# Performance work log

Measured on AMD Instinct MI355X. Metric: run time of the kernel, lower is better.

## Reference

```python
import jax, jax.numpy as jnp
import numpy as np

P, Q, R, H1, H2, PH, B = 32, 32, 8, 128, 64, 16, 8192
PAIRS = P * Q
OUT = PAIRS * R  # X_Z_layer output units


def _pairwise_mask(p, q, r):
    # rows i*q+k correspond to pair (x_i, z_k): connected to x_i and z_k only
    mx = np.zeros((p * q, p), np.float32)
    for i in range(p):
        mx[i * q:(i + 1) * q, i] = 1.0
    mz = np.tile(np.eye(q, dtype=np.float32), (p, 1))
    m = np.concatenate([mx, mz], axis=1)          # [p*q, p+q]
    return np.repeat(m, r, axis=0)                 # [p*q*r, p+q]


def setup_inputs() -> dict:
    key = jax.random.key(0)
    ks = jax.random.split(key, 24)
    rn = lambda k, s, sc=0.1: jax.random.normal(k, s, jnp.float32) * sc
    x = jax.random.normal(ks[0], (B, P), jnp.float32)
    z = jax.random.normal(ks[1], (B, Q), jnp.float32)
    # X_mlp: P -> H1 -> H2 -> 1
    xw1, xb1 = rn(ks[2], (P, H1)), rn(ks[3], (H1,))
    xw2, xb2 = rn(ks[4], (H1, H2)), rn(ks[5], (H2,))
    xw3, xb3 = rn(ks[6], (H2, 1)), rn(ks[7], (1,))
    # Z_mlp: Q -> H1 -> H2 -> 1
    zw1, zb1 = rn(ks[8], (Q, H1)), rn(ks[9], (H1,))
    zw2, zb2 = rn(ks[10], (Q if False else H1, H2)), rn(ks[11], (H2,))
    zw3, zb3 = rn(ks[12], (H2, 1)), rn(ks[13], (1,))
    # masked X_Z_layer: weight pre-multiplied by structured mask (as in __init__)
    mask = jnp.asarray(_pairwise_mask(P, Q, R))    # [OUT, P+Q]
    xzw = (rn(ks[14], (OUT, P + Q)) * mask).T      # [P+Q, OUT]
    xzb = rn(ks[15], (OUT,))
    # 1024 tiny per-pair MLPs: R -> PH (bias) -> 1 (no bias), stacked
    pw1 = rn(ks[16], (PAIRS, R, PH))
    pb1 = rn(ks[17], (PAIRS, PH))
    pw2 = rn(ks[18], (PAIRS, PH))
    return dict(x=x, z=z, xw1=xw1, xb1=xb1, xw2=xw2, xb2=xb2, xw3=xw3, xb3=xb3,
                zw1=zw1, zb1=zb1, zw2=zw2, zb2=zb2, zw3=zw3, zb3=zb3,
                xzw=xzw, xzb=xzb, pw1=pw1, pb1=pb1, pw2=pw2)


def reference(x, z, xw1, xb1, xw2, xb2, xw3, xb3,
              zw1, zb1, zw2, zb2, zw3, zb3, xzw, xzb, pw1, pb1, pw2):
    relu = jax.nn.relu
    # main-effect MLPs
    hx = relu(relu(x @ xw1 + xb1) @ xw2 + xb2)
    out_x = hx @ xw3 + xb3                         # [B,1]
    hz = relu(relu(z @ zw1 + zb1) @ zw2 + zb2)
    out_z = hz @ zw3 + zb3                         # [B,1]
    # masked interaction layer
    xz = jnp.concatenate([x, z], axis=1)           # [B, P+Q]
    h = relu(xz @ xzw + xzb)                       # [B, OUT]
    # all 1024 per-pair MLPs as one batched GEMM
    hp = h.reshape(h.shape[0], PAIRS, R)           # [B, pairs, R]
    t = relu(jnp.einsum('bpr,prh->bph', hp, pw1) + pb1)
    out_xz = jnp.einsum('bph,ph->b', t, pw2)[:, None]  # sum over pairs -> [B,1]
    return out_x + out_z + out_xz
```

## Files before the change

### kernel.cpp

```cpp
#include <hip/hip_runtime.h>

#define B_TOT 8192
#define PP 32
#define QQ 32
#define RR 8
#define H1 128
#define H2 64
#define PHH 16
#define PAIRS 1024
#define OUT_UNITS 8192

#define NBLK_MM 256
#define NBLK_IA 1024

typedef float f32x16 __attribute__((ext_vector_type(16)));
typedef short s16x8  __attribute__((ext_vector_type(8)));

union FragU { s16x8 v; unsigned int u[4]; };

__device__ inline unsigned int pack_bf16(float lo, float hi) {
    unsigned int r;
    asm("v_cvt_pk_bf16_f32 %0, %1, %2" : "=v"(r) : "v"(lo), "v"(hi));
    return r;
}

union SharedU {
    union {
        struct {
            float zT[16][256];
            float4 lwx[32][2];
            float4 lwz[32][2];
            float4 lhb[32][2];
            unsigned lpw1T[33][16][4];
            float lpbw[32][16][2];
        } s;
        float red[256][33];
    } ia;
    struct {
        union {
            float xT[32][68];
            float h1T[128][68];
        };
    } mm;
};

__global__ __launch_bounds__(512, 6) void fused_k(
    const float* __restrict__ x, const float* __restrict__ z,
    const float* __restrict__ xw1, const float* __restrict__ xb1,
    const float* __restrict__ xw2, const float* __restrict__ xb2,
    const float* __restrict__ xw3, const float* __restrict__ xb3,
    const float* __restrict__ zw1, const float* __restrict__ zb1,
    const float* __restrict__ zw2, const float* __restrict__ zb2,
    const float* __restrict__ zw3, const float* __restrict__ zb3,
    const float* __restrict__ xzw, const float* __restrict__ xzb,
    const float* __restrict__ pw1, const float* __restrict__ pb1,
    const float* __restrict__ pw2, float* __restrict__ out)
{
    __shared__ SharedU sh;
    const int bid  = blockIdx.x;
    const int t    = threadIdx.x;
    const int w    = t >> 6;
    const int lane = t & 63;

    if (bid >= NBLK_MM) {
        const int ib    = bid - NBLK_MM;
        const int bx    = ib & 31;
        const int y2    = ib >> 5;
        const int m     = lane & 31;
        const int kh    = lane >> 5;
        const int jj    = m & 15;
        const int cph   = m >> 4;
        const int b0    = bx * 256;
        const int par   = y2 & 1;
        const int i_xb  = y2 & ~1;
        const int k0    = par * 16;
        const int oy0   = 2 * i_xb + par;
        const int oy1   = oy0 + 2;
        const int pair0_0 = oy0 * 16;
        const int pair0_1 = oy1 * 16;

        {
            int row = t >> 1;
            int c8  = (t & 1) * 8;
            const float* src = z + (size_t)(b0 + row) * 32 + k0 + c8;
            float4 a4 = *reinterpret_cast<const float4*>(src);
            float4 b4 = *reinterpret_cast<const float4*>(src + 4);
            sh.ia.s.zT[c8+0][row] = a4.x; sh.ia.s.zT[c8+1][row] = a4.y;
            sh.ia.s.zT[c8+2][row] = a4.z; sh.ia.s.zT[c8+3][row] = a4.w;
            sh.ia.s.zT[c8+4][row] = b4.x; sh.ia.s.zT[c8+5][row] = b4.y;
            sh.ia.s.zT[c8+6][row] = b4.z; sh.ia.s.zT[c8+7][row] = b4.w;
        }
        if (t < 256) {
            int sb  = t >> 7;
            int idx = t & 127;
            int p = idx >> 3, c = idx & 7;
            int gp = (sb ? pair0_1 : pair0_0) + p;
            int pl = sb * 16 + p;
            reinterpret_cast<float*>(sh.ia.s.lwx)[pl*8 + c] = xzw[(size_t)(i_xb + sb) * OUT_UNITS + gp*8 + c];
            reinterpret_cast<float*>(sh.ia.s.lwz)[pl*8 + c] = xzw[(size_t)(32 + k0 + p) * OUT_UNITS + gp*8 + c];
            reinterpret_cast<float*>(sh.ia.s.lhb)[pl*8 + c] = xzb[gp*8 + c];
        }
        {
            int p = t >> 4, j = t & 15;
            int gp = ((p >> 4) ? pair0_1 : pair0_0) + (p & 15);
            float2 bw;
            bw.x = pb1[gp*PHH + j];
            bw.y = pw2[gp*PHH + j];
            *reinterpret_cast<float2*>(sh.ia.s.lpbw[p][j]) = bw;
        }
        #pragma unroll
        for (int it = 0; it < 4; ++it) {
            int idx = t + it * 512;
            int p = idx >> 6, u = (idx >> 4) & 3, j = idx & 15;
            int gp = ((p >> 4) ? pair0_1 : pair0_0) + (p & 15);
            float lo = pw1[(size_t)gp * 128 + (2*u)*16 + j];
            float hi = pw1[(size_t)gp * 128 + (2*u+1)*16 + j];
            sh.ia.s.lpw1T[p][j][u] = pack_bf16(lo, hi);
        }
        if (t < 64) reinterpret_cast<unsigned*>(sh.ia.s.lpw1T[32])[t] = 0u;

        const int bl = w * 32 + m;
        const float2 xv2 = *reinterpret_cast<const float2*>(
            x + (size_t)(b0 + bl) * 32 + i_xb);
        __syncthreads();

        f32x16 acc;
        #pragma unroll
        for (int r = 0; r < 16; ++r) acc[r] = 0.f;

        const bool realB = (kh == cph);

        #pragma unroll 2
        for (int ppl = 0; ppl < 8; ++ppl) {
            const int kA = 2*ppl + kh;
            const int kB = 2*ppl + cph;
            const float zv = sh.ia.s.zT[kA][bl];

            #pragma unroll
            for (int sb = 0; sb < 2; ++sb) {
                const int pAl = sb*16 + kA;
                const int pBl = sb*16 + kB;
                const float xv = sb ? xv2.y : xv2.x;

                const float4 wxa = sh.ia.s.lwx[pAl][0], wxb = sh.ia.s.lwx[pAl][1];
                const float4 wza = sh.ia.s.lwz[pAl][0], wzb = sh.ia.s.lwz[pAl][1];
                const float4 hba = sh.ia.s.lhb[pAl][0], hbb = sh.ia.s.lhb[pAl][1];

                float h0[8];
                h0[0] = fmaxf(fmaf(xv, wxa.x, fmaf(zv, wza.x, hba.x)), 0.f);
                h0[1] = fmaxf(fmaf(xv, wxa.y, fmaf(zv, wza.y, hba.y)), 0.f);
                h0[2] = fmaxf(fmaf(xv, wxa.z, fmaf(zv, wza.z, hba.z)), 0.f);
                h0[3] = fmaxf(fmaf(xv, wxa.w, fmaf(zv, wza.w, hba.w)), 0.f);
                h0[4] = fmaxf(fmaf(xv, wxb.x, fmaf(zv, wzb.x, hbb.x)), 0.f);
                h0[5] = fmaxf(fmaf(xv, wxb.y, fmaf(zv, wzb.y, hbb.y)), 0.f);
                h0[6] = fmaxf(fmaf(xv, wxb.z, fmaf(zv, wzb.z, hbb.z)), 0.f);
                h0[7] = fmaxf(fmaf(xv, wxb.w, fmaf(zv, wzb.w, hbb.w)), 0.f);

                FragU a0, bf;
                a0.u[0] = pack_bf16(h0[0], h0[1]);
                a0.u[1] = pack_bf16(h0[2], h0[3]);
                a0.u[2] = pack_bf16(h0[4], h0[5]);
                a0.u[3] = pack_bf16(h0[6], h0[7]);

                const unsigned* bq = sh.ia.s.lpw1T[realB ? pBl : 32][jj];
                bf.u[0] = bq[0]; bf.u[1] = bq[1]; bf.u[2] = bq[2]; bf.u[3] = bq[3];

                const float2 bw = *reinterpret_cast<const float2*>(sh.ia.s.lpbw[pBl][jj]);

                f32x16 cpb;
                #pragma unroll
                for (int r = 0; r < 16; ++r) cpb[r] = bw.x;

                f32x16 d = __builtin_amdgcn_mfma_f32_32x32x16_bf16(a0.v, bf.v, cpb, 0, 0, 0);

                #pragma unroll
                for (int r = 0; r < 16; ++r)
                    acc[r] = fmaf(fmaxf(d[r], 0.f), bw.y, acc[r]);
            }
        }

        __syncthreads();
        #pragma unroll
        for (int r = 0; r < 16; ++r) {
            int rowf = (r & 3) + 8 * (r >> 2) + 4 * kh;
            sh.ia.red[w * 32 + rowf][m] = acc[r];
        }
        __syncthreads();
        {
            int row = t >> 1, hh = t & 1;
            const float* rr = &sh.ia.red[row][hh * 16];
            float ssum = 0.f;
            #pragma unroll
            for (int c = 0; c < 16; ++c) ssum += rr[c];
            ssum += __shfl_xor(ssum, 1);
            if (hh == 0) atomicAdd(out + b0 + row, ssum);
        }
    } else {
        const int btile = bid & 127;
        const int which = bid >> 7;
        const float* in = which ? z   : x;
        const float* w1 = which ? zw1 : xw1;
        const float* b1 = which ? zb1 : xb1;
        const float* w2 = which ? zw2 : xw2;
        const float* b2 = which ? zb2 : xb2;
        const float* w3 = which ? zw3 : xw3;
        const float* b3 = which ? zb3 : xb3;
        const int b0 = btile * 64;
        const int bw = w * 8;

        {
            int row = t >> 3;
            int c4  = (t & 7) * 4;
            float4 v = *reinterpret_cast<const float4*>(in + (size_t)(b0 + row) * 32 + c4);
            sh.mm.xT[c4+0][row] = v.x; sh.mm.xT[c4+1][row] = v.y;
            sh.mm.xT[c4+2][row] = v.z; sh.mm.xT[c4+3][row] = v.w;
        }
        __syncthreads();

        const int j1 = lane, j2 = lane + 64;
        float a1[8], a2[8];
        {
            float bb1 = b1[j1], bb2 = b1[j2];
            #pragma unroll
            for (int i = 0; i < 8; ++i) { a1[i] = bb1; a2[i] = bb2; }
        }
        #pragma unroll 4
        for (int m = 0; m < 32; ++m) {
            const float4* xr = reinterpret_cast<const float4*>(&sh.mm.xT[m][bw]);
            float4 xa = xr[0], xb = xr[1];
            float wv1 = w1[m*H1 + j1];
            float wv2 = w1[m*H1 + j2];
            a1[0] = fmaf(xa.x, wv1, a1[0]); a2[0] = fmaf(xa.x, wv2, a2[0]);
            a1[1] = fmaf(xa.y, wv1, a1[1]); a2[1] = fmaf(xa.y, wv2, a2[1]);
            a1[2] = fmaf(xa.z, wv1, a1[2]); a2[2] = fmaf(xa.z, wv2, a2[2]);
            a1[3] = fmaf(xa.w, wv1, a1[3]); a2[3] = fmaf(xa.w, wv2, a2[3]);
            a1[4] = fmaf(xb.x, wv1, a1[4]); a2[4] = fmaf(xb.x, wv2, a2[4]);
            a1[5] = fmaf(xb.y, wv1, a1[5]); a2[5] = fmaf(xb.y, wv2, a2[5]);
            a1[6] = fmaf(xb.z, wv1, a1[6]); a2[6] = fmaf(xb.z, wv2, a2[6]);
            a1[7] = fmaf(xb.w, wv1, a1[7]); a2[7] = fmaf(xb.w, wv2, a2[7]);
        }
        __syncthreads();
        #pragma unroll
        for (int i = 0; i < 8; ++i) {
            sh.mm.h1T[j1][bw + i] = fmaxf(a1[i], 0.f);
            sh.mm.h1T[j2][bw + i] = fmaxf(a2[i], 0.f);
        }
        __syncthreads();

        float hacc[8];
        {
            float b2v = b2[lane];
            #pragma unroll
            for (int i = 0; i < 8; ++i) hacc[i] = b2v;
        }
        #pragma unroll 4
        for (int m = 0; m < 128; ++m) {
            float w2v = w2[m*H2 + lane];
            const float4* hr = reinterpret_cast<const float4*>(&sh.mm.h1T[m][bw]);
            float4 ha = hr[0], hb = hr[1];
            hacc[0] = fmaf(ha.x, w2v, hacc[0]);
            hacc[1] = fmaf(ha.y, w2v, hacc[1]);
            hacc[2] = fmaf(ha.z, w2v, hacc[2]);
            hacc[3] = fmaf(ha.w, w2v, hacc[3]);
            hacc[4] = fmaf(hb.x, w2v, hacc[4]);
            hacc[5] = fmaf(hb.y, w2v, hacc[5]);
            hacc[6] = fmaf(hb.z, w2v, hacc[6]);
            hacc[7] = fmaf(hb.w, w2v, hacc[7]);
        }
        {
            float w3v = w3[lane];
            #pragma unroll
            for (int i = 0; i < 8; ++i) hacc[i] = fmaxf(hacc[i], 0.f) * w3v;
        }
        __syncthreads();
        #pragma unroll
        for (int i = 0; i < 8; ++i)
            sh.mm.h1T[bw + i][lane] = hacc[i];
        __syncthreads();
        if (t < 64) {
            float s = b3[0];
            const float4* rr = reinterpret_cast<const float4*>(&sh.mm.h1T[t][0]);
            #pragma unroll
            for (int c = 0; c < 16; ++c) {
                float4 v = rr[c];
                s += (v.x + v.y) + (v.z + v.w);
            }
            atomicAdd(out + b0 + t, s);
        }
    }
}

extern "C" void kernel_launch(void* const* d_in, const int* in_sizes, int n_in,
                              void* d_out, int out_size, void* d_ws, size_t ws_size,
                              hipStream_t stream) {
    const float* x   = (const float*)d_in[0];
    const float* z   = (const float*)d_in[1];
    const float* xw1 = (const float*)d_in[2];
    const float* xb1 = (const float*)d_in[3];
    const float* xw2 = (const float*)d_in[4];
    const float* xb2 = (const float*)d_in[5];
    const float* xw3 = (const float*)d_in[6];
    const float* xb3 = (const float*)d_in[7];
    const float* zw1 = (const float*)d_in[8];
    const float* zb1 = (const float*)d_in[9];
    const float* zw2 = (const float*)d_in[10];
    const float* zb2 = (const float*)d_in[11];
    const float* zw3 = (const float*)d_in[12];
    const float* zb3 = (const float*)d_in[13];
    const float* xzw = (const float*)d_in[14];
    const float* xzb = (const float*)d_in[15];
    const float* pw1 = (const float*)d_in[16];
    const float* pb1 = (const float*)d_in[17];
    const float* pw2 = (const float*)d_in[18];
    float* out = (float*)d_out;

    hipMemsetAsync(out, 0, (size_t)out_size * sizeof(float), stream);

    fused_k<<<dim3(NBLK_MM + NBLK_IA), 512, 0, stream>>>(
        x, z, xw1, xb1, xw2, xb2, xw3, xb3,
        zw1, zb1, zw2, zb2, zw3, zb3,
        xzw, xzb, pw1, pb1, pw2, out);
}
```

Before: 117.3 us.

## Process four x-rows per interaction block, halving the interaction block count

Each interaction block now covers four x indices (64 pairs) instead of two, so only half as many interaction blocks are launched. The z transpose staging and the per-block setup and reduction are amortized over twice the pair work. In exchange the shared-memory staging of weights doubles, the inner loop runs four sub-blocks per iteration with unrolling reduced, and fewer blocks are available to fill the GPU.

```diff
diff --git a/kernel.cpp b/kernel.cpp
--- a/kernel.cpp
+++ b/kernel.cpp
@@ -11,7 +11,7 @@
 #define OUT_UNITS 8192
 
 #define NBLK_MM 256
-#define NBLK_IA 1024
+#define NBLK_IA 512
 
 typedef float f32x16 __attribute__((ext_vector_type(16)));
 typedef short s16x8  __attribute__((ext_vector_type(8)));
@@ -28,11 +28,11 @@
     union {
         struct {
             float zT[16][256];
-            float4 lwx[32][2];
-            float4 lwz[32][2];
-            float4 lhb[32][2];
-            unsigned lpw1T[33][16][4];
-            float lpbw[32][16][2];
+            float4 lwx[64][2];
+            float4 lwz[64][2];
+            float4 lhb[64][2];
+            unsigned lpw1T[65][16][4];
+            float lpbw[64][16][2];
         } s;
         float red[256][33];
     } ia;
@@ -65,19 +65,15 @@
     if (bid >= NBLK_MM) {
         const int ib    = bid - NBLK_MM;
         const int bx    = ib & 31;
-        const int y2    = ib >> 5;
+        const int y4    = ib >> 5;
         const int m     = lane & 31;
         const int kh    = lane >> 5;
         const int jj    = m & 15;
         const int cph   = m >> 4;
         const int b0    = bx * 256;
-        const int par   = y2 & 1;
-        const int i_xb  = y2 & ~1;
+        const int par   = y4 & 1;
+        const int i_xb  = (y4 >> 1) * 4;
         const int k0    = par * 16;
-        const int oy0   = 2 * i_xb + par;
-        const int oy1   = oy0 + 2;
-        const int pair0_0 = oy0 * 16;
-        const int pair0_1 = oy1 * 16;
 
         {
             int row = t >> 1;
@@ -90,37 +86,38 @@
             sh.ia.s.zT[c8+4][row] = b4.x; sh.ia.s.zT[c8+5][row] = b4.y;
             sh.ia.s.zT[c8+6][row] = b4.z; sh.ia.s.zT[c8+7][row] = b4.w;
         }
-        if (t < 256) {
-            int sb  = t >> 7;
-            int idx = t & 127;
-            int p = idx >> 3, c = idx & 7;
-            int gp = (sb ? pair0_1 : pair0_0) + p;
-            int pl = sb * 16 + p;
-            reinterpret_cast<float*>(sh.ia.s.lwx)[pl*8 + c] = xzw[(size_t)(i_xb + sb) * OUT_UNITS + gp*8 + c];
+        {
+            int pl = t >> 3, c = t & 7;
+            int s  = pl >> 4, p = pl & 15;
+            int ix = i_xb + s;
+            int gp = 32*ix + 16*par + p;
+            reinterpret_cast<float*>(sh.ia.s.lwx)[pl*8 + c] = xzw[(size_t)ix * OUT_UNITS + gp*8 + c];
             reinterpret_cast<float*>(sh.ia.s.lwz)[pl*8 + c] = xzw[(size_t)(32 + k0 + p) * OUT_UNITS + gp*8 + c];
             reinterpret_cast<float*>(sh.ia.s.lhb)[pl*8 + c] = xzb[gp*8 + c];
         }
-        {
-            int p = t >> 4, j = t & 15;
-            int gp = ((p >> 4) ? pair0_1 : pair0_0) + (p & 15);
+        #pragma unroll
+        for (int it = 0; it < 2; ++it) {
+            int idx = t + it * 512;
+            int p = idx >> 4, j = idx & 15;
+            int gp = 32*(i_xb + (p >> 4)) + 16*par + (p & 15);
             float2 bw;
             bw.x = pb1[gp*PHH + j];
             bw.y = pw2[gp*PHH + j];
             *reinterpret_cast<float2*>(sh.ia.s.lpbw[p][j]) = bw;
         }
         #pragma unroll
-        for (int it = 0; it < 4; ++it) {
+        for (int it = 0; it < 8; ++it) {
             int idx = t + it * 512;
             int p = idx >> 6, u = (idx >> 4) & 3, j = idx & 15;
-            int gp = ((p >> 4) ? pair0_1 : pair0_0) + (p & 15);
+            int gp = 32*(i_xb + (p >> 4)) + 16*par + (p & 15);
             float lo = pw1[(size_t)gp * 128 + (2*u)*16 + j];
             float hi = pw1[(size_t)gp * 128 + (2*u+1)*16 + j];
             sh.ia.s.lpw1T[p][j][u] = pack_bf16(lo, hi);
         }
-        if (t < 64) reinterpret_cast<unsigned*>(sh.ia.s.lpw1T[32])[t] = 0u;
+        if (t < 64) reinterpret_cast<unsigned*>(sh.ia.s.lpw1T[64])[t] = 0u;
 
         const int bl = w * 32 + m;
-        const float2 xv2 = *reinterpret_cast<const float2*>(
+        const float4 xv4 = *reinterpret_cast<const float4*>(
             x + (size_t)(b0 + bl) * 32 + i_xb);
         __syncthreads();
 
@@ -130,17 +127,18 @@
 
         const bool realB = (kh == cph);
 
-        #pragma unroll 2
+        #pragma unroll 1
         for (int ppl = 0; ppl < 8; ++ppl) {
             const int kA = 2*ppl + kh;
             const int kB = 2*ppl + cph;
             const float zv = sh.ia.s.zT[kA][bl];
 
             #pragma unroll
-            for (int sb = 0; sb < 2; ++sb) {
+            for (int sb = 0; sb < 4; ++sb) {
                 const int pAl = sb*16 + kA;
                 const int pBl = sb*16 + kB;
-                const float xv = sb ? xv2.y : xv2.x;
+                const float xv = (sb == 0) ? xv4.x : (sb == 1) ? xv4.y
+                               : (sb == 2) ? xv4.z : xv4.w;
 
                 const float4 wxa = sh.ia.s.lwx[pAl][0], wxb = sh.ia.s.lwx[pAl][1];
                 const float4 wza = sh.ia.s.lwz[pAl][0], wzb = sh.ia.s.lwz[pAl][1];
@@ -162,7 +160,7 @@
                 a0.u[2] = pack_bf16(h0[4], h0[5]);
                 a0.u[3] = pack_bf16(h0[6], h0[7]);
 
-                const unsigned* bq = sh.ia.s.lpw1T[realB ? pBl : 32][jj];
+                const unsigned* bq = sh.ia.s.lpw1T[realB ? pBl : 64][jj];
                 bf.u[0] = bq[0]; bf.u[1] = bq[1]; bf.u[2] = bq[2]; bf.u[3] = bq[3];
 
                 const float2 bw = *reinterpret_cast<const float2*>(sh.ia.s.lpbw[pBl][jj]);
```

Measured after the change: 190.8 us. 62.7% more time.
